# Kernel optimization log

Hardware: AMD Instinct MI355X
Metric: run time of the kernel (lower is better)

The kernel has to match this reference:

```python
import math
import jax, jax.numpy as jnp
import numpy as np

N, E, H, D, NNZ = 32768, 512, 8, 64, 524288


def setup_inputs() -> dict:
    key = jax.random.key(0)
    ks = jax.random.split(key, 12)
    x = jax.random.normal(ks[0], (N, E), dtype=jnp.float32)
    row_index = jnp.sort(jax.random.randint(ks[1], (NNZ,), 0, N))
    col_index = jax.random.randint(ks[2], (NNZ,), 0, N)
    to_col_index = jax.random.randint(ks[3], (N,), 0, N)
    att_bias = jax.random.normal(ks[4], (H, NNZ), dtype=jnp.float32)
    # positive interatomic distances in ~[0.5, 5.5)
    dist = jax.random.uniform(ks[5], (NNZ,), dtype=jnp.float32) * 5.0 + 0.5
    pos = jax.random.normal(ks[6], (N, 3), dtype=jnp.float32)
    col_pos = jax.random.normal(ks[7], (N, 3), dtype=jnp.float32)
    s = 1.0 / math.sqrt(E)
    q_w = jax.random.normal(ks[8], (E, E), dtype=jnp.float32) * s
    q_b = jax.random.normal(ks[9], (E,), dtype=jnp.float32) * 0.02
    k_w = jax.random.normal(ks[10], (E, E), dtype=jnp.float32) * s
    k_b = jax.random.normal(ks[11], (E,), dtype=jnp.float32) * 0.02
    return {"x": x, "row_index": row_index, "col_index": col_index,
            "to_col_index": to_col_index, "att_bias": att_bias, "dist": dist,
            "pos": pos, "col_pos": col_pos,
            "q_w": q_w, "q_b": q_b, "k_w": k_w, "k_b": k_b}


def reference(x, row_index, col_index, to_col_index, att_bias, dist, pos, col_pos,
              q_w, q_b, k_w, k_b):
    n = x.shape[0]
    h = att_bias.shape[0]
    d = x.shape[1] // h
    # per-head projections: [N, H, D]
    q = (x @ q_w.T + q_b).reshape(n, h, d) * (1.0 / math.sqrt(d))
    k = (x @ k_w.T + k_b).reshape(n, h, d)[to_col_index]  # [Nk, H, D]
    # sparse (COO) masked q @ k^T plus additive bias -> per-edge logits [nnz, H]
    logits = jnp.einsum('ehd,ehd->eh', q[row_index], k[col_index]) + att_bias.T
    # sparse softmax over each query row (per head)
    m = jax.ops.segment_max(logits, row_index, num_segments=n)       # [N, H]
    p = jnp.exp(logits - m[row_index])
    z = jax.ops.segment_sum(p, row_index, num_segments=n)            # [N, H]
    att = p / z[row_index]                                           # [nnz, H]
    # distance-weighted attention (dist==0 -> contribution 0, as x/inf in torch)
    inv_d = jnp.where(dist == 0, 0.0, 1.0 / dist)
    att = att * inv_d[:, None]
    # sparse bmm against col_pos values and against ones
    cp = col_pos[col_index]                                          # [nnz, 3]
    dst_vec = jax.ops.segment_sum(att[:, :, None] * cp[:, None, :],
                                  row_index, num_segments=n)         # [N, H, 3]
    avg_inv_dist = jax.ops.segment_sum(att, row_index, num_segments=n)  # [N, H]
    src_vec = avg_inv_dist[..., None] * pos[:, None, :]              # [N, H, 3]
    v = dst_vec - src_vec
    norm = jnp.sqrt(jnp.sum(v * v, axis=-1, keepdims=True))
    feat3 = v / jnp.maximum(norm, 1e-12)                             # F.normalize
    feat = jnp.concatenate([feat3, avg_inv_dist[..., None]], axis=-1)  # [N, H, 4]
    return feat.reshape(n, h * 4)
```

## Files before the change

kernel.cpp:

```cpp
#include <hip/hip_runtime.h>
#include <math.h>
#include <stdint.h>

#define N_NODES 32768
#define E_DIM   512
#define H_HEADS 8
#define D_HEAD  64
#define NNZ_E   524288

typedef __attribute__((ext_vector_type(4))) float f32x4;
typedef __attribute__((ext_vector_type(8))) _Float16 f16x8;
typedef __attribute__((ext_vector_type(2))) _Float16 f16x2;

__device__ __forceinline__ void async16(const void* g, void* l) {
  __builtin_amdgcn_global_load_lds(
      (const __attribute__((address_space(1))) void*)g,
      (__attribute__((address_space(3))) void*)l, 16, 0, 0);
}

__device__ __forceinline__ float dot8(const f16x8 a, const f16x8 b, float acc) {
#if __has_builtin(__builtin_amdgcn_fdot2)
  acc = __builtin_amdgcn_fdot2(__builtin_shufflevector(a, a, 0, 1),
                               __builtin_shufflevector(b, b, 0, 1), acc, false);
  acc = __builtin_amdgcn_fdot2(__builtin_shufflevector(a, a, 2, 3),
                               __builtin_shufflevector(b, b, 2, 3), acc, false);
  acc = __builtin_amdgcn_fdot2(__builtin_shufflevector(a, a, 4, 5),
                               __builtin_shufflevector(b, b, 4, 5), acc, false);
  acc = __builtin_amdgcn_fdot2(__builtin_shufflevector(a, a, 6, 7),
                               __builtin_shufflevector(b, b, 6, 7), acc, false);
#else
#pragma unroll
  for (int i = 0; i < 8; ++i) acc = fmaf((float)a[i], (float)b[i], acc);
#endif
  return acc;
}

__global__ __launch_bounds__(256) void prep_small(
    const float* __restrict__ x,
    const float* __restrict__ q_w, const float* __restrict__ k_w,
    const int* __restrict__ row_index, const int* __restrict__ col_index,
    const int* __restrict__ to_col,
    _Float16* __restrict__ wq_h, _Float16* __restrict__ wk_h,
    _Float16* __restrict__ xs,
    int* __restrict__ row_start, int* __restrict__ ge) {
  const int b = blockIdx.x;
  if (b < 8448) {
    const float* src;
    _Float16* dst;
    int t;
    if (b < 128)      { src = q_w; dst = wq_h; t = b * 256 + threadIdx.x; }
    else if (b < 256) { src = k_w; dst = wk_h; t = (b - 128) * 256 + threadIdx.x; }
    else              { src = x;   dst = xs;   t = (b - 256) * 256 + threadIdx.x; }
    const int r = t >> 6;
    const int c8 = (t & 63) << 3;
    const float4 v0 = *(const float4*)(src + (size_t)r * 512 + c8);
    const float4 v1 = *(const float4*)(src + (size_t)r * 512 + c8 + 4);
    f16x8 o;
    o[0] = (_Float16)v0.x; o[1] = (_Float16)v0.y;
    o[2] = (_Float16)v0.z; o[3] = (_Float16)v0.w;
    o[4] = (_Float16)v1.x; o[5] = (_Float16)v1.y;
    o[6] = (_Float16)v1.z; o[7] = (_Float16)v1.w;
    *(f16x8*)(dst + (size_t)r * 512 + c8) = o;
  } else {
    const int e = (b - 8448) * 256 + threadIdx.x;
    if (e < NNZ_E) {
      ge[e] = to_col[col_index[e]];
      const int r0 = row_index[e];
      const int r1 = (e + 1 < NNZ_E) ? row_index[e + 1] : N_NODES;
      if (e == 0)
        for (int r = 0; r <= r0; ++r) row_start[r] = 0;
      for (int r = r0 + 1; r <= r1; ++r) row_start[r] = e + 1;
    }
  }
}

__global__ __launch_bounds__(256) void gemm_mfma(
    const _Float16* __restrict__ xs,
    const _Float16* __restrict__ wqh,
    const _Float16* __restrict__ wkh,
    const float* __restrict__ q_b, const float* __restrict__ k_b,
    _Float16* __restrict__ qh, _Float16* __restrict__ kh) {
  __shared__ _Float16 Ah0[128 * 32];
  __shared__ _Float16 Ah1[128 * 32];
  __shared__ _Float16 Bh0[128 * 32];
  __shared__ _Float16 Bh1[128 * 32];
  const int tid = threadIdx.x;
  const int w = tid >> 6;
  const int l = tid & 63;

  const int b = blockIdx.x;
  const int j = b >> 3;
  const int mb = (b & 7) * 32 + (j >> 3);
  const int c = j & 7;
  const bool is_q = ((c & 1) == 0);
  const int bm = mb * 128;
  const int bn = (c >> 1) * 128;

  const _Float16* __restrict__ wmat = is_q ? wqh : wkh;
  const float* __restrict__ bias = is_q ? q_b : k_b;
  _Float16* __restrict__ outp = is_q ? qh : kh;
  const float oscale = is_q ? 0.125f : 1.0f;

  const int wm = (w & 1) * 64;
  const int wn = (w >> 1) * 64;

  f32x4 acc[4][4];
#pragma unroll
  for (int i = 0; i < 4; ++i)
#pragma unroll
    for (int jj = 0; jj < 4; ++jj) acc[i][jj] = (f32x4){0.f, 0.f, 0.f, 0.f};

  const int sr0 = w * 16 + (l >> 2);
  const int sr1 = sr0 + 64;
  const int sc = (((l & 3) ^ ((l >> 3) & 3)) << 3);
  const int fr = l & 15;
  const int fcs = ((((l >> 4) ^ ((fr >> 1) & 3)) & 3) << 3);

  const _Float16* __restrict__ wa = wmat + (size_t)bn * 512;
  const _Float16* __restrict__ xa = xs + (size_t)bm * 512;

  for (int k0 = 0; k0 < 512; k0 += 64) {
    async16(xa + (size_t)sr0 * 512 + k0 + sc, Ah0 + w * 512);
    async16(xa + (size_t)sr1 * 512 + k0 + sc, Ah0 + (w + 4) * 512);
    async16(xa + (size_t)sr0 * 512 + k0 + 32 + sc, Ah1 + w * 512);
    async16(xa + (size_t)sr1 * 512 + k0 + 32 + sc, Ah1 + (w + 4) * 512);
    async16(wa + (size_t)sr0 * 512 + k0 + sc, Bh0 + w * 512);
    async16(wa + (size_t)sr1 * 512 + k0 + sc, Bh0 + (w + 4) * 512);
    async16(wa + (size_t)sr0 * 512 + k0 + 32 + sc, Bh1 + w * 512);
    async16(wa + (size_t)sr1 * 512 + k0 + 32 + sc, Bh1 + (w + 4) * 512);
    __syncthreads();

    f16x8 av0[4], av1[4], bv0[4], bv1[4];
#pragma unroll
    for (int i = 0; i < 4; ++i) {
      const int ro = (wm + i * 16 + fr) * 32 + fcs;
      av0[i] = *(const f16x8*)(Ah0 + ro);
      av1[i] = *(const f16x8*)(Ah1 + ro);
    }
#pragma unroll
    for (int i = 0; i < 4; ++i) {
      const int ro = (wn + i * 16 + fr) * 32 + fcs;
      bv0[i] = *(const f16x8*)(Bh0 + ro);
      bv1[i] = *(const f16x8*)(Bh1 + ro);
    }
#pragma unroll
    for (int i = 0; i < 4; ++i)
#pragma unroll
      for (int jj = 0; jj < 4; ++jj)
        acc[i][jj] = __builtin_amdgcn_mfma_f32_16x16x32_f16(
            av0[i], bv0[jj], acc[i][jj], 0, 0, 0);
#pragma unroll
    for (int i = 0; i < 4; ++i)
#pragma unroll
      for (int jj = 0; jj < 4; ++jj)
        acc[i][jj] = __builtin_amdgcn_mfma_f32_16x16x32_f16(
            av1[i], bv1[jj], acc[i][jj], 0, 0, 0);
    __syncthreads();
  }

  const int cn = l & 15;
  const int cm4 = (l >> 4) * 4;
  float bvals[4];
#pragma unroll
  for (int jj = 0; jj < 4; ++jj) bvals[jj] = bias[bn + wn + jj * 16 + cn];
#pragma unroll
  for (int i = 0; i < 4; ++i) {
#pragma unroll
    for (int r = 0; r < 4; ++r) {
      const int m = bm + wm + i * 16 + cm4 + r;
      _Float16* op = outp + (size_t)m * 512 + bn + wn + cn;
#pragma unroll
      for (int jj = 0; jj < 4; ++jj) {
        op[jj * 16] = (_Float16)((acc[i][jj][r] + bvals[jj]) * oscale);
      }
    }
  }
}

__global__ __launch_bounds__(256) void row_fused(
    const _Float16* __restrict__ qh, const _Float16* __restrict__ kh,
    const int* __restrict__ row_start, const int* __restrict__ ge,
    const float* __restrict__ att_bias, const int* __restrict__ col_index,
    const float* __restrict__ dist, const float* __restrict__ pos,
    const float* __restrict__ col_pos, float* __restrict__ out) {
  const int r = blockIdx.x * 4 + (threadIdx.x >> 6);
  const int lane = threadIdx.x & 63;
  const int h = lane >> 3;
  const int start = row_start[r];
  const int end = row_start[r + 1];

  const f16x8 qv = *(const f16x8*)(qh + (size_t)r * E_DIM + lane * 8);
  const float* __restrict__ biasp = att_bias + (size_t)h * NNZ_E;

  float m = -INFINITY, l = 0.f, accw = 0.f, a0 = 0.f, a1 = 0.f, a2 = 0.f;

  auto edge_logit = [&](const f16x8 kv) -> float {
    float s = dot8(qv, kv, 0.f);
    s += __shfl_xor(s, 1);
    s += __shfl_xor(s, 2);
    s += __shfl_xor(s, 4);
    return s;
  };
  auto upd = [&](float logit, float dd, float c0, float c1, float c2) {
    const float w = (dd == 0.f) ? 0.f : __builtin_amdgcn_rcpf(dd);
    const float nm = fmaxf(m, logit);
    const float sc = __expf(m - nm);
    const float p = __expf(logit - nm);
    m = nm;
    l = fmaf(l, sc, p);
    const float pw = p * w;
    accw = fmaf(accw, sc, pw);
    a0 = fmaf(a0, sc, pw * c0);
    a1 = fmaf(a1, sc, pw * c1);
    a2 = fmaf(a2, sc, pw * c2);
  };

  int e = start;
  for (; e + 4 <= end; e += 4) {
    int g[4], cc[4];
    float dd[4], bb[4], cp[4][3];
    f16x8 kv[4];
#pragma unroll
    for (int i = 0; i < 4; ++i) g[i] = ge[e + i];
#pragma unroll
    for (int i = 0; i < 4; ++i)
      kv[i] = *(const f16x8*)(kh + (size_t)g[i] * E_DIM + lane * 8);
#pragma unroll
    for (int i = 0; i < 4; ++i) {
      cc[i] = col_index[e + i];
      dd[i] = dist[e + i];
      bb[i] = biasp[e + i];
    }
#pragma unroll
    for (int i = 0; i < 4; ++i) {
      cp[i][0] = col_pos[cc[i] * 3 + 0];
      cp[i][1] = col_pos[cc[i] * 3 + 1];
      cp[i][2] = col_pos[cc[i] * 3 + 2];
    }
    float s[4];
#pragma unroll
    for (int i = 0; i < 4; ++i) s[i] = edge_logit(kv[i]) + bb[i];
#pragma unroll
    for (int i = 0; i < 4; ++i) upd(s[i], dd[i], cp[i][0], cp[i][1], cp[i][2]);
  }
  for (; e < end; ++e) {
    const int g0 = ge[e];
    const f16x8 kv0 = *(const f16x8*)(kh + (size_t)g0 * E_DIM + lane * 8);
    const int c0 = col_index[e];
    const float dd0 = dist[e];
    const float bb0 = biasp[e];
    const float cp00 = col_pos[c0 * 3 + 0];
    const float cp01 = col_pos[c0 * 3 + 1];
    const float cp02 = col_pos[c0 * 3 + 2];
    const float s0 = edge_logit(kv0) + bb0;
    upd(s0, dd0, cp00, cp01, cp02);
  }

  if ((lane & 7) == 0) {
    const float invz = (l > 0.f) ? 1.f / l : 0.f;
    const float avg = accw * invz;
    const float v0 = a0 * invz - avg * pos[r * 3 + 0];
    const float v1 = a1 * invz - avg * pos[r * 3 + 1];
    const float v2 = a2 * invz - avg * pos[r * 3 + 2];
    const float nrm = sqrtf(v0 * v0 + v1 * v1 + v2 * v2);
    const float invn = 1.f / fmaxf(nrm, 1e-12f);
    float4 o;
    o.x = v0 * invn; o.y = v1 * invn; o.z = v2 * invn; o.w = avg;
    *(float4*)(out + (size_t)r * (H_HEADS * 4) + h * 4) = o;
  }
}

extern "C" void kernel_launch(void* const* d_in, const int* in_sizes, int n_in,
                              void* d_out, int out_size, void* d_ws,
                              size_t ws_size, hipStream_t stream) {
  const float* x        = (const float*)d_in[0];
  const int* row_index  = (const int*)d_in[1];
  const int* col_index  = (const int*)d_in[2];
  const int* to_col     = (const int*)d_in[3];
  const float* att_bias = (const float*)d_in[4];
  const float* dist     = (const float*)d_in[5];
  const float* pos      = (const float*)d_in[6];
  const float* col_pos  = (const float*)d_in[7];
  const float* q_w      = (const float*)d_in[8];
  const float* q_b      = (const float*)d_in[9];
  const float* k_w      = (const float*)d_in[10];
  const float* k_b      = (const float*)d_in[11];
  float* out = (float*)d_out;

  _Float16* qh = (_Float16*)d_ws;
  _Float16* kh = qh + (size_t)N_NODES * 512;
  _Float16* xs = kh + (size_t)N_NODES * 512;
  _Float16* wq_h = xs + (size_t)N_NODES * 512;
  _Float16* wk_h = wq_h + 512 * 512;
  int* row_start = (int*)(wk_h + 512 * 512);
  int* ge = row_start + (N_NODES + 1);

  prep_small<<<8448 + NNZ_E / 256, 256, 0, stream>>>(
      x, q_w, k_w, row_index, col_index, to_col, wq_h, wk_h, xs, row_start, ge);

  gemm_mfma<<<2048, 256, 0, stream>>>(xs, wq_h, wk_h, q_b, k_b, qh, kh);

  row_fused<<<N_NODES / 4, 256, 0, stream>>>(qh, kh, row_start, ge, att_bias,
                                             col_index, dist, pos, col_pos,
                                             out);
}
```

Baseline: 262.9 us.

## Fuse x fp32-to-fp16 conversion into GEMM tile loads

Drops the separate prepass that converted x to an fp16 workspace copy. The GEMM now stages fp32 x tiles into LDS with a swizzled layout and converts them to fp16 while building the MFMA operands. The K step shrinks from 64 to 32 to fit the fp32 tile, which doubles the number of loop iterations and barriers. The aim is to remove the extra global read and write of x, at the cost of more per-iteration sync and conversion work inside the GEMM.

```diff
diff --git a/kernel.cpp b/kernel.cpp
--- a/kernel.cpp
+++ b/kernel.cpp
@@ -10,7 +10,6 @@
 
 typedef __attribute__((ext_vector_type(4))) float f32x4;
 typedef __attribute__((ext_vector_type(8))) _Float16 f16x8;
-typedef __attribute__((ext_vector_type(2))) _Float16 f16x2;
 
 __device__ __forceinline__ void async16(const void* g, void* l) {
   __builtin_amdgcn_global_load_lds(
@@ -36,21 +35,16 @@
 }
 
 __global__ __launch_bounds__(256) void prep_small(
-    const float* __restrict__ x,
     const float* __restrict__ q_w, const float* __restrict__ k_w,
     const int* __restrict__ row_index, const int* __restrict__ col_index,
     const int* __restrict__ to_col,
     _Float16* __restrict__ wq_h, _Float16* __restrict__ wk_h,
-    _Float16* __restrict__ xs,
     int* __restrict__ row_start, int* __restrict__ ge) {
   const int b = blockIdx.x;
-  if (b < 8448) {
-    const float* src;
-    _Float16* dst;
-    int t;
-    if (b < 128)      { src = q_w; dst = wq_h; t = b * 256 + threadIdx.x; }
-    else if (b < 256) { src = k_w; dst = wk_h; t = (b - 128) * 256 + threadIdx.x; }
-    else              { src = x;   dst = xs;   t = (b - 256) * 256 + threadIdx.x; }
+  if (b < 256) {
+    const float* src = (b < 128) ? q_w : k_w;
+    _Float16* dst = (b < 128) ? wq_h : wk_h;
+    const int t = (b & 127) * 256 + threadIdx.x;
     const int r = t >> 6;
     const int c8 = (t & 63) << 3;
     const float4 v0 = *(const float4*)(src + (size_t)r * 512 + c8);
@@ -62,7 +56,7 @@
     o[6] = (_Float16)v1.z; o[7] = (_Float16)v1.w;
     *(f16x8*)(dst + (size_t)r * 512 + c8) = o;
   } else {
-    const int e = (b - 8448) * 256 + threadIdx.x;
+    const int e = (b - 256) * 256 + threadIdx.x;
     if (e < NNZ_E) {
       ge[e] = to_col[col_index[e]];
       const int r0 = row_index[e];
@@ -75,15 +69,13 @@
 }
 
 __global__ __launch_bounds__(256) void gemm_mfma(
-    const _Float16* __restrict__ xs,
+    const float* __restrict__ x,
     const _Float16* __restrict__ wqh,
     const _Float16* __restrict__ wkh,
     const float* __restrict__ q_b, const float* __restrict__ k_b,
     _Float16* __restrict__ qh, _Float16* __restrict__ kh) {
-  __shared__ _Float16 Ah0[128 * 32];
-  __shared__ _Float16 Ah1[128 * 32];
-  __shared__ _Float16 Bh0[128 * 32];
-  __shared__ _Float16 Bh1[128 * 32];
+  __shared__ float Af[128 * 32];
+  __shared__ _Float16 Bh[128 * 32];
   const int tid = threadIdx.x;
   const int w = tid >> 6;
   const int l = tid & 63;
@@ -110,51 +102,51 @@
 #pragma unroll
     for (int jj = 0; jj < 4; ++jj) acc[i][jj] = (f32x4){0.f, 0.f, 0.f, 0.f};
 
+  const int ar = l >> 3;
+  const int agc = (l & 7) ^ ar;
   const int sr0 = w * 16 + (l >> 2);
   const int sr1 = sr0 + 64;
   const int sc = (((l & 3) ^ ((l >> 3) & 3)) << 3);
   const int fr = l & 15;
   const int fcs = ((((l >> 4) ^ ((fr >> 1) & 3)) & 3) << 3);
+  const int akc = (l >> 4) * 2;
+  const int as = l & 7;
 
   const _Float16* __restrict__ wa = wmat + (size_t)bn * 512;
-  const _Float16* __restrict__ xa = xs + (size_t)bm * 512;
-
-  for (int k0 = 0; k0 < 512; k0 += 64) {
-    async16(xa + (size_t)sr0 * 512 + k0 + sc, Ah0 + w * 512);
-    async16(xa + (size_t)sr1 * 512 + k0 + sc, Ah0 + (w + 4) * 512);
-    async16(xa + (size_t)sr0 * 512 + k0 + 32 + sc, Ah1 + w * 512);
-    async16(xa + (size_t)sr1 * 512 + k0 + 32 + sc, Ah1 + (w + 4) * 512);
-    async16(wa + (size_t)sr0 * 512 + k0 + sc, Bh0 + w * 512);
-    async16(wa + (size_t)sr1 * 512 + k0 + sc, Bh0 + (w + 4) * 512);
-    async16(wa + (size_t)sr0 * 512 + k0 + 32 + sc, Bh1 + w * 512);
-    async16(wa + (size_t)sr1 * 512 + k0 + 32 + sc, Bh1 + (w + 4) * 512);
+
+  for (int k0 = 0; k0 < 512; k0 += 32) {
+#pragma unroll
+    for (int cc = 0; cc < 4; ++cc) {
+      const int rbase = cc * 32 + w * 8;
+      async16(x + (size_t)(bm + rbase + ar) * 512 + k0 + agc * 4,
+              Af + rbase * 32);
+    }
+    async16(wa + (size_t)sr0 * 512 + k0 + sc, Bh + w * 512);
+    async16(wa + (size_t)sr1 * 512 + k0 + sc, Bh + (w + 4) * 512);
     __syncthreads();
 
-    f16x8 av0[4], av1[4], bv0[4], bv1[4];
+    f16x8 av[4], bv[4];
 #pragma unroll
     for (int i = 0; i < 4; ++i) {
-      const int ro = (wm + i * 16 + fr) * 32 + fcs;
-      av0[i] = *(const f16x8*)(Ah0 + ro);
-      av1[i] = *(const f16x8*)(Ah1 + ro);
-    }
-#pragma unroll
-    for (int i = 0; i < 4; ++i) {
-      const int ro = (wn + i * 16 + fr) * 32 + fcs;
-      bv0[i] = *(const f16x8*)(Bh0 + ro);
-      bv1[i] = *(const f16x8*)(Bh1 + ro);
-    }
+      const float* rp = Af + (wm + i * 16 + fr) * 32;
+      const float4 fa = *(const float4*)(rp + ((akc ^ as) << 2));
+      const float4 fb = *(const float4*)(rp + (((akc + 1) ^ as) << 2));
+      f16x8 v;
+      v[0] = (_Float16)fa.x; v[1] = (_Float16)fa.y;
+      v[2] = (_Float16)fa.z; v[3] = (_Float16)fa.w;
+      v[4] = (_Float16)fb.x; v[5] = (_Float16)fb.y;
+      v[6] = (_Float16)fb.z; v[7] = (_Float16)fb.w;
+      av[i] = v;
+    }
+#pragma unroll
+    for (int i = 0; i < 4; ++i)
+      bv[i] = *(const f16x8*)(Bh + (wn + i * 16 + fr) * 32 + fcs);
 #pragma unroll
     for (int i = 0; i < 4; ++i)
 #pragma unroll
       for (int jj = 0; jj < 4; ++jj)
         acc[i][jj] = __builtin_amdgcn_mfma_f32_16x16x32_f16(
-            av0[i], bv0[jj], acc[i][jj], 0, 0, 0);
-#pragma unroll
-    for (int i = 0; i < 4; ++i)
-#pragma unroll
-      for (int jj = 0; jj < 4; ++jj)
-        acc[i][jj] = __builtin_amdgcn_mfma_f32_16x16x32_f16(
-            av1[i], bv1[jj], acc[i][jj], 0, 0, 0);
+            av[i], bv[jj], acc[i][jj], 0, 0, 0);
     __syncthreads();
   }
 
@@ -289,16 +281,15 @@
 
   _Float16* qh = (_Float16*)d_ws;
   _Float16* kh = qh + (size_t)N_NODES * 512;
-  _Float16* xs = kh + (size_t)N_NODES * 512;
-  _Float16* wq_h = xs + (size_t)N_NODES * 512;
+  _Float16* wq_h = kh + (size_t)N_NODES * 512;
   _Float16* wk_h = wq_h + 512 * 512;
   int* row_start = (int*)(wk_h + 512 * 512);
   int* ge = row_start + (N_NODES + 1);
 
-  prep_small<<<8448 + NNZ_E / 256, 256, 0, stream>>>(
-      x, q_w, k_w, row_index, col_index, to_col, wq_h, wk_h, xs, row_start, ge);
-
-  gemm_mfma<<<2048, 256, 0, stream>>>(xs, wq_h, wk_h, q_b, k_b, qh, kh);
+  prep_small<<<256 + NNZ_E / 256, 256, 0, stream>>>(
+      q_w, k_w, row_index, col_index, to_col, wq_h, wk_h, row_start, ge);
+
+  gemm_mfma<<<2048, 256, 0, stream>>>(x, wq_h, wk_h, q_b, k_b, qh, kh);
 
   row_fused<<<N_NODES / 4, 256, 0, stream>>>(qh, kh, row_start, ge, att_bias,
                                              col_index, dist, pos, col_pos,
```

Result: slower. 283.3 us (+7.8%).
